# Optimization experiments

Hardware: AMD Instinct MI355X
Metric: run time of the kernel (lower is better)

## Reference

```python
import jax, jax.numpy as jnp
import numpy as np

N_NODES = 50000
N_EDGES = 800000
IN_DIM = 1024
HID = 512          # hidden_channels * heads, heads=1
N_CLASSES = 6
N_GRAPHS = 8
NEG_SLOPE = 0.2    # PyG GATConv default LeakyReLU slope
EPS = 1e-16


def gat_conv(x, W, att_src, att_dst, bias, src, dst):
    """PyG GATConv with heads=1, concat=True.
    x: [N, Fin], W: [Fin, C], att_src/att_dst: [C], bias: [C],
    src/dst: [E] (edge_index[0], edge_index[1]); messages flow src -> dst.
    """
    h = x @ W                                   # [N, C]
    a_s = h @ att_src                           # [N]
    a_d = h @ att_dst                           # [N]
    e = jax.nn.leaky_relu(a_s[src] + a_d[dst], NEG_SLOPE)   # [E]
    # segment softmax over destination node
    m = jax.ops.segment_max(e, dst, num_segments=N_NODES)   # [N]
    ex = jnp.exp(e - m[dst])                                 # [E]
    denom = jax.ops.segment_sum(ex, dst, num_segments=N_NODES)  # [N]
    alpha = ex / (denom[dst] + EPS)                           # [E]
    msg = alpha[:, None] * h[src]                             # [E, C]
    out = jax.ops.segment_sum(msg, dst, num_segments=N_NODES)  # [N, C]
    return out + bias


def setup_inputs() -> dict:
    key = jax.random.key(0)
    ks = jax.random.split(key, 20)
    x = jax.random.normal(ks[0], (N_NODES, IN_DIM), dtype=jnp.float32)
    edge_index = jax.random.randint(ks[1], (2, N_EDGES), 0, N_NODES, dtype=jnp.int32)
    batch = jnp.sort(jax.random.randint(ks[2], (N_NODES,), 0, N_GRAPHS, dtype=jnp.int32))

    def glorot(k, shape):
        fan = shape[0] + shape[-1]
        return jax.random.normal(k, shape, dtype=jnp.float32) * jnp.sqrt(2.0 / fan)

    inp = {"x": x, "edge_index": edge_index, "batch": batch}
    dims = [(IN_DIM, HID), (HID, HID), (HID, HID)]
    for i, (fi, fo) in enumerate(dims, start=1):
        inp[f"W{i}"] = glorot(ks[3 * i], (fi, fo))
        inp[f"as{i}"] = glorot(ks[3 * i + 1], (fo,))
        inp[f"ad{i}"] = glorot(ks[3 * i + 2], (fo,))
        inp[f"b{i}"] = jnp.zeros((fo,), dtype=jnp.float32)
    inp["Wlin"] = glorot(ks[13], (HID, N_CLASSES))
    inp["blin"] = jnp.zeros((N_CLASSES,), dtype=jnp.float32)
    return inp


def reference(x, W1, as1, ad1, b1, W2, as2, ad2, b2, W3, as3, ad3, b3,
              Wlin, blin, edge_index, batch):
    src, dst = edge_index[0], edge_index[1]
    h = gat_conv(x, W1, as1, ad1, b1, src, dst)
    h = jax.nn.relu(h)
    h = gat_conv(h, W2, as2, ad2, b2, src, dst)
    h = jax.nn.relu(h)
    h = gat_conv(h, W3, as3, ad3, b3, src, dst)
    # global_max_pool over graphs; dropout is identity in eval mode
    pooled = jax.ops.segment_max(h, batch, num_segments=N_GRAPHS)  # [G, HID]
    return pooled @ Wlin + blin                                     # [G, num_classes]
```

## Files before the change

kernel.cpp:

```cpp
#include <hip/hip_runtime.h>
#include <cmath>

#define N_NODES 50000
#define N_EDGES 800000
#define IN_DIM 1024
#define HID 512
#define N_CLASSES 6
#define N_GRAPHS 8
#define NEG_SLOPE 0.2f
#define SCAN_BLK 256
#define N_SCAN_BLOCKS ((N_NODES + SCAN_BLK - 1) / SCAN_BLK)
#define POOL_STRIP 256
#define POOL_NBLOCKS ((N_NODES + POOL_STRIP - 1) / POOL_STRIP)

typedef _Float16 half8 __attribute__((ext_vector_type(8)));
typedef _Float16 half4 __attribute__((ext_vector_type(4)));
typedef float floatx4 __attribute__((ext_vector_type(4)));

typedef const __attribute__((address_space(1))) void* gas_ptr;
typedef __attribute__((address_space(3))) void* las_ptr;
#define GLOAD16(gp, lp) \
    __builtin_amdgcn_global_load_lds((gas_ptr)(gp), (las_ptr)(lp), 16, 0, 0)

__global__ __launch_bounds__(256) void cast_x_f16(const float* __restrict__ x,
                                                  _Float16* __restrict__ x16) {
    const size_t TOT = (size_t)N_NODES * IN_DIM;
    size_t i = ((size_t)blockIdx.x * blockDim.x + threadIdx.x) * 8;
    const size_t step = (size_t)gridDim.x * blockDim.x * 8;
    for (; i < TOT; i += step) {
        float4 f0 = *(const float4*)(x + i);
        float4 f1 = *(const float4*)(x + i + 4);
        half8 o;
        o[0] = (_Float16)f0.x; o[1] = (_Float16)f0.y;
        o[2] = (_Float16)f0.z; o[3] = (_Float16)f0.w;
        o[4] = (_Float16)f1.x; o[5] = (_Float16)f1.y;
        o[6] = (_Float16)f1.z; o[7] = (_Float16)f1.w;
        *(half8*)(x16 + i) = o;
    }
}

__global__ __launch_bounds__(256) void transpose_cast_W3(const float* __restrict__ W1,
                                                         const float* __restrict__ W2,
                                                         const float* __restrict__ W3,
                                                         _Float16* __restrict__ Wt1,
                                                         _Float16* __restrict__ Wt2,
                                                         _Float16* __restrict__ Wt3) {
    const int l = blockIdx.z;
    const float* W = (l == 0) ? W1 : (l == 1) ? W2 : W3;
    _Float16* Wt   = (l == 0) ? Wt1 : (l == 1) ? Wt2 : Wt3;
    const int K    = (l == 0) ? IN_DIM : HID;
    if (blockIdx.x * 32 >= K) return;
    __shared__ float sh[32][33];
    const int kb = blockIdx.x * 32, nb = blockIdx.y * 32;
    const int tx = threadIdx.x & 31, ty = threadIdx.x >> 5;
#pragma unroll
    for (int i = 0; i < 32; i += 8)
        sh[ty + i][tx] = W[(size_t)(kb + ty + i) * HID + nb + tx];
    __syncthreads();
#pragma unroll
    for (int i = 0; i < 32; i += 8)
        Wt[(size_t)(nb + ty + i) * K + kb + tx] = (_Float16)sh[tx][ty + i];
}

__global__ __launch_bounds__(256) void gemm_mfma_f16(const _Float16* __restrict__ A,
                                                     const _Float16* __restrict__ Bt,
                                                     _Float16* __restrict__ C,
                                                     int M, int K) {
    const int nwg = gridDim.x;
    const int bid = blockIdx.x;
    const int q = nwg >> 3, r = nwg & 7;
    const int xcd = bid & 7, local = bid >> 3;
    const int wgid = (xcd < r) ? xcd * (q + 1) + local
                               : r * (q + 1) + (xcd - r) * q + local;
    const int rowBase = (wgid >> 2) * 128;
    const int colBase = (wgid & 3) * 128;

    const int tid  = threadIdx.x;
    const int lane = tid & 63;
    const int wave = tid >> 6;
    const int wm = wave >> 1, wn = wave & 1;

    __shared__ __align__(16) _Float16 As[128 * 64];
    __shared__ __align__(16) _Float16 Bs[128 * 64];

    const int fr = lane & 15;
    const int kc = lane >> 4;

    floatx4 acc[4][4] = {};

    const int lrow   = lane >> 3;
    const int gchunk = ((lane & 7) ^ lrow) * 8;
    const _Float16* aS[4];
    const _Float16* bS[4];
    _Float16* aD[4];
    _Float16* bD[4];
#pragma unroll
    for (int i = 0; i < 4; ++i) {
        int rr = wave * 32 + i * 8;
        int ar = rowBase + rr + lrow; if (ar > M - 1) ar = M - 1;
        aS[i] = A  + (size_t)ar * K + gchunk;
        bS[i] = Bt + (size_t)(colBase + rr + lrow) * K + gchunk;
        aD[i] = As + rr * 64;
        bD[i] = Bs + rr * 64;
    }

    const int cp0 = ((kc)     ^ (fr & 7)) * 8;
    const int cp1 = ((4 + kc) ^ (fr & 7)) * 8;
    const int aro = (wm * 64 + fr) * 64;
    const int bro = (wn * 64 + fr) * 64;

    for (int kb = 0; kb < K; kb += 64) {
#pragma unroll
        for (int i = 0; i < 4; ++i) {
            GLOAD16(aS[i] + kb, aD[i]);
            GLOAD16(bS[i] + kb, bD[i]);
        }
        __syncthreads();

#pragma unroll
        for (int kks = 0; kks < 2; ++kks) {
            const int cp = kks ? cp1 : cp0;
            half8 afr[4], bfr[4];
#pragma unroll
            for (int mi = 0; mi < 4; ++mi)
                afr[mi] = *(const half8*)&As[aro + mi * 1024 + cp];
#pragma unroll
            for (int ni = 0; ni < 4; ++ni)
                bfr[ni] = *(const half8*)&Bs[bro + ni * 1024 + cp];
#pragma unroll
            for (int mi = 0; mi < 4; ++mi)
#pragma unroll
                for (int ni = 0; ni < 4; ++ni)
                    acc[mi][ni] = __builtin_amdgcn_mfma_f32_16x16x32_f16(
                        afr[mi], bfr[ni], acc[mi][ni], 0, 0, 0);
        }
        __syncthreads();
    }

#pragma unroll
    for (int mi = 0; mi < 4; ++mi) {
#pragma unroll
        for (int ni = 0; ni < 4; ++ni) {
            int col = colBase + wn * 64 + ni * 16 + fr;
#pragma unroll
            for (int j = 0; j < 4; ++j) {
                int row = rowBase + wm * 64 + mi * 16 + kc * 4 + j;
                if (row < M) C[(size_t)row * HID + col] = (_Float16)acc[mi][ni][j];
            }
        }
    }
}

__global__ __launch_bounds__(256) void adot_kernel(const _Float16* __restrict__ h,
                                                   const float* __restrict__ att_s,
                                                   const float* __restrict__ att_d,
                                                   float* __restrict__ a_s,
                                                   float* __restrict__ a_d) {
    int wave = threadIdx.x >> 6;
    int lane = threadIdx.x & 63;
    int n = blockIdx.x * 4 + wave;
    if (n >= N_NODES) return;
    half8 hv = *(const half8*)(h + (size_t)n * HID + lane * 8);
    float4 s0 = ((const float4*)att_s)[lane * 2];
    float4 s1 = ((const float4*)att_s)[lane * 2 + 1];
    float4 d0 = ((const float4*)att_d)[lane * 2];
    float4 d1 = ((const float4*)att_d)[lane * 2 + 1];
    float hf[8];
#pragma unroll
    for (int q = 0; q < 8; ++q) hf[q] = (float)hv[q];
    float ss = hf[0]*s0.x + hf[1]*s0.y + hf[2]*s0.z + hf[3]*s0.w
             + hf[4]*s1.x + hf[5]*s1.y + hf[6]*s1.z + hf[7]*s1.w;
    float sd = hf[0]*d0.x + hf[1]*d0.y + hf[2]*d0.z + hf[3]*d0.w
             + hf[4]*d1.x + hf[5]*d1.y + hf[6]*d1.z + hf[7]*d1.w;
#pragma unroll
    for (int off = 32; off; off >>= 1) {
        ss += __shfl_down(ss, off);
        sd += __shfl_down(sd, off);
    }
    if (lane == 0) { a_s[n] = ss; a_d[n] = sd; }
}

__global__ void count_kernel(const int* __restrict__ dst, int* __restrict__ cnt) {
    int i = blockIdx.x * blockDim.x + threadIdx.x;
    if (i < N_EDGES) atomicAdd(cnt + dst[i], 1);
}

__global__ __launch_bounds__(SCAN_BLK) void scan1_kernel(const int* __restrict__ cnt,
                                                         int* __restrict__ partial,
                                                         int* __restrict__ blocksum) {
    __shared__ int tmp[SCAN_BLK];
    int t = threadIdx.x;
    int i = blockIdx.x * SCAN_BLK + t;
    int v = (i < N_NODES) ? cnt[i] : 0;
    tmp[t] = v;
    __syncthreads();
    for (int off = 1; off < SCAN_BLK; off <<= 1) {
        int u = (t >= off) ? tmp[t - off] : 0;
        __syncthreads();
        tmp[t] += u;
        __syncthreads();
    }
    if (i < N_NODES) partial[i] = tmp[t] - v;
    if (t == SCAN_BLK - 1) blocksum[blockIdx.x] = tmp[t];
}

__global__ __launch_bounds__(SCAN_BLK) void scan2_kernel(int* __restrict__ blocksum) {
    __shared__ int tmp[SCAN_BLK];
    int t = threadIdx.x;
    int v = (t < N_SCAN_BLOCKS) ? blocksum[t] : 0;
    tmp[t] = v;
    __syncthreads();
    for (int off = 1; off < SCAN_BLK; off <<= 1) {
        int u = (t >= off) ? tmp[t - off] : 0;
        __syncthreads();
        tmp[t] += u;
        __syncthreads();
    }
    if (t < N_SCAN_BLOCKS) blocksum[t] = tmp[t] - v;
}

__global__ __launch_bounds__(SCAN_BLK) void scan3_kernel(const int* __restrict__ partial,
                                                         const int* __restrict__ blocksum,
                                                         int* __restrict__ rowptr,
                                                         int* __restrict__ cursor) {
    int i = blockIdx.x * SCAN_BLK + threadIdx.x;
    if (i < N_NODES) {
        int r = partial[i] + blocksum[blockIdx.x];
        rowptr[i] = r;
        cursor[i] = r;
    }
    if (i == 0) rowptr[N_NODES] = N_EDGES;
}

__global__ void scatter_kernel(const int* __restrict__ src, const int* __restrict__ dst,
                               int* __restrict__ cursor, int* __restrict__ src_s) {
    int i = blockIdx.x * blockDim.x + threadIdx.x;
    if (i >= N_EDGES) return;
    int p = atomicAdd(cursor + dst[i], 1);
    src_s[p] = src[i];
}

__global__ __launch_bounds__(256) void alpha_kernel(const int* __restrict__ rowptr,
                                                    const int* __restrict__ src_s,
                                                    const float* __restrict__ a_s,
                                                    const float* __restrict__ a_d,
                                                    float* __restrict__ alpha) {
    const int grp = threadIdx.x >> 4;
    const int l16 = threadIdx.x & 15;
    const int n = blockIdx.x * 16 + grp;
    if (n >= N_NODES) return;
    const int beg = rowptr[n], end = rowptr[n + 1];
    const float a_dn = a_d[n];

    float vmax = -__builtin_inff();
    for (int j = beg + l16; j < end; j += 16) {
        float v = a_s[src_s[j]] + a_dn;
        v = v > 0.f ? v : NEG_SLOPE * v;
        alpha[j] = v;
        vmax = fmaxf(vmax, v);
    }
#pragma unroll
    for (int m = 1; m < 16; m <<= 1) vmax = fmaxf(vmax, __shfl_xor(vmax, m));

    float psum = 0.f;
    for (int j = beg + l16; j < end; j += 16) {
        float p = __expf(alpha[j] - vmax);
        alpha[j] = p;
        psum += p;
    }
#pragma unroll
    for (int m = 1; m < 16; m <<= 1) psum += __shfl_xor(psum, m);

    const float inv = 1.f / (psum + 1e-16f);
    for (int j = beg + l16; j < end; j += 16) alpha[j] *= inv;
}

__global__ __launch_bounds__(256) void aggregate2(const int* __restrict__ rowptr,
                                                  const int* __restrict__ src_s,
                                                  const float* __restrict__ alpha,
                                                  const _Float16* __restrict__ h,
                                                  const float* __restrict__ bias,
                                                  int do_relu,
                                                  _Float16* __restrict__ outx) {
    int wave = threadIdx.x >> 6;
    int lane = threadIdx.x & 63;
    int n = blockIdx.x * 4 + wave;
    if (n >= N_NODES) return;
    const int beg = rowptr[n], end = rowptr[n + 1];
    float acc[8] = {};
    int j = beg;
    for (; j + 1 < end; j += 2) {
        int s0 = src_s[j], s1 = src_s[j + 1];
        float al0 = alpha[j], al1 = alpha[j + 1];
        half8 hv0 = *(const half8*)(h + (size_t)s0 * HID + lane * 8);
        half8 hv1 = *(const half8*)(h + (size_t)s1 * HID + lane * 8);
#pragma unroll
        for (int q = 0; q < 8; ++q) acc[q] = fmaf(al0, (float)hv0[q], acc[q]);
#pragma unroll
        for (int q = 0; q < 8; ++q) acc[q] = fmaf(al1, (float)hv1[q], acc[q]);
    }
    if (j < end) {
        int s0 = src_s[j];
        float al0 = alpha[j];
        half8 hv0 = *(const half8*)(h + (size_t)s0 * HID + lane * 8);
#pragma unroll
        for (int q = 0; q < 8; ++q) acc[q] = fmaf(al0, (float)hv0[q], acc[q]);
    }
    const float4 b0 = ((const float4*)(bias + lane * 8))[0];
    const float4 b1 = ((const float4*)(bias + lane * 8))[1];
    float o[8];
    o[0] = acc[0] + b0.x; o[1] = acc[1] + b0.y;
    o[2] = acc[2] + b0.z; o[3] = acc[3] + b0.w;
    o[4] = acc[4] + b1.x; o[5] = acc[5] + b1.y;
    o[6] = acc[6] + b1.z; o[7] = acc[7] + b1.w;
    half8 ov;
#pragma unroll
    for (int q = 0; q < 8; ++q) {
        float val = do_relu ? fmaxf(o[q], 0.f) : o[q];
        ov[q] = (_Float16)val;
    }
    *(half8*)(outx + (size_t)n * HID + lane * 8) = ov;
}

__global__ __launch_bounds__(128) void pool1_kernel(const _Float16* __restrict__ X,
                                                    const int* __restrict__ batch,
                                                    float* __restrict__ partial) {
    const int t = threadIdx.x;
    const int b = blockIdx.x;
    const int n0 = b * POOL_STRIP;
    const int n1 = min(n0 + POOL_STRIP, N_NODES);
    const float NEG = -__builtin_inff();
    const float4 neg4 = make_float4(NEG, NEG, NEG, NEG);
#pragma unroll
    for (int g = 0; g < N_GRAPHS; ++g)
        ((float4*)(partial + ((size_t)b * N_GRAPHS + g) * HID))[t] = neg4;
    int gcur = batch[n0];
    float4 m = neg4;
    for (int n = n0; n < n1; ++n) {
        int g = batch[n];
        if (g != gcur) {
            ((float4*)(partial + ((size_t)b * N_GRAPHS + gcur) * HID))[t] = m;
            m = neg4;
            gcur = g;
        }
        half4 hv = *(const half4*)(X + (size_t)n * HID + t * 4);
        m.x = fmaxf(m.x, (float)hv[0]); m.y = fmaxf(m.y, (float)hv[1]);
        m.z = fmaxf(m.z, (float)hv[2]); m.w = fmaxf(m.w, (float)hv[3]);
    }
    ((float4*)(partial + ((size_t)b * N_GRAPHS + gcur) * HID))[t] = m;
}

__global__ __launch_bounds__(128) void pool2_kernel(const float* __restrict__ partial,
                                                    float* __restrict__ pooled) {
    const int g = blockIdx.x;
    const int t = threadIdx.x;
    const float NEG = -__builtin_inff();
    float4 m = make_float4(NEG, NEG, NEG, NEG);
    for (int b = 0; b < POOL_NBLOCKS; ++b) {
        float4 v = ((const float4*)(partial + ((size_t)b * N_GRAPHS + g) * HID))[t];
        m.x = fmaxf(m.x, v.x); m.y = fmaxf(m.y, v.y);
        m.z = fmaxf(m.z, v.z); m.w = fmaxf(m.w, v.w);
    }
    ((float4*)(pooled + (size_t)g * HID))[t] = m;
}

__global__ __launch_bounds__(64) void final_linear_kernel(const float* __restrict__ pooled,
                                                          const float* __restrict__ Wlin,
                                                          const float* __restrict__ blin,
                                                          float* __restrict__ out) {
    int t = threadIdx.x;
    if (t >= N_GRAPHS * N_CLASSES) return;
    int g = t / N_CLASSES, c = t % N_CLASSES;
    float s = blin[c];
    for (int k = 0; k < HID; ++k)
        s = fmaf(pooled[(size_t)g * HID + k], Wlin[(size_t)k * N_CLASSES + c], s);
    out[t] = s;
}

extern "C" void kernel_launch(void* const* d_in, const int* in_sizes, int n_in,
                              void* d_out, int out_size, void* d_ws, size_t ws_size,
                              hipStream_t stream) {
    const float* x       = (const float*)d_in[0];
    const int*   eidx    = (const int*)d_in[1];
    const int*   batch   = (const int*)d_in[2];
    const float* W[3]    = {(const float*)d_in[3], (const float*)d_in[7], (const float*)d_in[11]};
    const float* Asrc[3] = {(const float*)d_in[4], (const float*)d_in[8], (const float*)d_in[12]};
    const float* Adst[3] = {(const float*)d_in[5], (const float*)d_in[9], (const float*)d_in[13]};
    const float* Bias[3] = {(const float*)d_in[6], (const float*)d_in[10], (const float*)d_in[14]};
    const float* Wlin    = (const float*)d_in[15];
    const float* blin    = (const float*)d_in[16];
    const int* src = eidx;
    const int* dst = eidx + N_EDGES;

    float* wsf    = (float*)d_ws;
    _Float16* x16 = (_Float16*)wsf;
    float* ealpha = wsf + 24800000;
    _Float16* hH  = (_Float16*)(wsf + 25600000);
    _Float16* xAct= (_Float16*)(wsf + 25600000 + 12800000);
    float* a_s    = wsf + 25600000 + 12800000 + 12800000;
    float* a_d    = a_s + N_NODES;
    float* pooled = a_d + N_NODES;
    int* cnt      = (int*)(pooled + N_GRAPHS * HID);
    int* rowptr   = cnt + N_NODES;
    int* cursor   = rowptr + N_NODES + 1;
    int* partial  = cursor + N_NODES;
    int* blocksum = partial + N_NODES;
    int* src_s    = blocksum + 256;
    _Float16* Wt1 = (_Float16*)(src_s + N_EDGES);
    _Float16* Wt2 = Wt1 + (size_t)HID * IN_DIM;
    _Float16* Wt3 = Wt2 + (size_t)HID * HID;
    _Float16* WtL[3] = {Wt1, Wt2, Wt3};

    int edge_blocks = (N_EDGES + 255) / 256;

    hipMemsetAsync(cnt, 0, N_NODES * sizeof(int), stream);
    count_kernel<<<edge_blocks, 256, 0, stream>>>(dst, cnt);
    scan1_kernel<<<N_SCAN_BLOCKS, SCAN_BLK, 0, stream>>>(cnt, partial, blocksum);
    scan2_kernel<<<1, SCAN_BLK, 0, stream>>>(blocksum);
    scan3_kernel<<<N_SCAN_BLOCKS, SCAN_BLK, 0, stream>>>(partial, blocksum, rowptr, cursor);
    scatter_kernel<<<edge_blocks, 256, 0, stream>>>(src, dst, cursor, src_s);

    cast_x_f16<<<2048, 256, 0, stream>>>(x, x16);
    dim3 tgrid(IN_DIM / 32, HID / 32, 3);
    transpose_cast_W3<<<tgrid, 256, 0, stream>>>(W[0], W[1], W[2], Wt1, Wt2, Wt3);

    const int nrow_tiles = (N_NODES + 127) / 128;
    const int gemm_blocks = nrow_tiles * (HID / 128);
    for (int l = 0; l < 3; ++l) {
        int K = (l == 0) ? IN_DIM : HID;
        const _Float16* Ain = (l == 0) ? x16 : xAct;
        gemm_mfma_f16<<<gemm_blocks, 256, 0, stream>>>(Ain, WtL[l], hH, N_NODES, K);
        adot_kernel<<<(N_NODES + 3) / 4, 256, 0, stream>>>(hH, Asrc[l], Adst[l], a_s, a_d);
        alpha_kernel<<<(N_NODES + 15) / 16, 256, 0, stream>>>(rowptr, src_s, a_s, a_d, ealpha);
        aggregate2<<<(N_NODES + 3) / 4, 256, 0, stream>>>(
            rowptr, src_s, ealpha, hH, Bias[l], (l < 2) ? 1 : 0, xAct);
    }

    float* pool_partial = (float*)x16;
    pool1_kernel<<<POOL_NBLOCKS, 128, 0, stream>>>(xAct, batch, pool_partial);
    pool2_kernel<<<N_GRAPHS, 128, 0, stream>>>(pool_partial, pooled);
    final_linear_kernel<<<1, 64, 0, stream>>>(pooled, Wlin, blin, (float*)d_out);
}
```

Before: 830.3 us.

## Fuse attention dot products into GEMM epilogue and unroll aggregation by four

```diff
diff --git a/kernel.cpp b/kernel.cpp
--- a/kernel.cpp
+++ b/kernel.cpp
@@ -65,6 +65,10 @@
 __global__ __launch_bounds__(256) void gemm_mfma_f16(const _Float16* __restrict__ A,
                                                      const _Float16* __restrict__ Bt,
                                                      _Float16* __restrict__ C,
+                                                     const float* __restrict__ att_s,
+                                                     const float* __restrict__ att_d,
+                                                     float* __restrict__ a_s,
+                                                     float* __restrict__ a_d,
                                                      int M, int K) {
     const int nwg = gridDim.x;
     const int bid = blockIdx.x;
@@ -149,35 +153,36 @@
             }
         }
     }
-}
-
-__global__ __launch_bounds__(256) void adot_kernel(const _Float16* __restrict__ h,
-                                                   const float* __restrict__ att_s,
-                                                   const float* __restrict__ att_d,
-                                                   float* __restrict__ a_s,
-                                                   float* __restrict__ a_d) {
-    int wave = threadIdx.x >> 6;
-    int lane = threadIdx.x & 63;
-    int n = blockIdx.x * 4 + wave;
-    if (n >= N_NODES) return;
-    half8 hv = *(const half8*)(h + (size_t)n * HID + lane * 8);
-    float4 s0 = ((const float4*)att_s)[lane * 2];
-    float4 s1 = ((const float4*)att_s)[lane * 2 + 1];
-    float4 d0 = ((const float4*)att_d)[lane * 2];
-    float4 d1 = ((const float4*)att_d)[lane * 2 + 1];
-    float hf[8];
-#pragma unroll
-    for (int q = 0; q < 8; ++q) hf[q] = (float)hv[q];
-    float ss = hf[0]*s0.x + hf[1]*s0.y + hf[2]*s0.z + hf[3]*s0.w
-             + hf[4]*s1.x + hf[5]*s1.y + hf[6]*s1.z + hf[7]*s1.w;
-    float sd = hf[0]*d0.x + hf[1]*d0.y + hf[2]*d0.z + hf[3]*d0.w
-             + hf[4]*d1.x + hf[5]*d1.y + hf[6]*d1.z + hf[7]*d1.w;
-#pragma unroll
-    for (int off = 32; off; off >>= 1) {
-        ss += __shfl_down(ss, off);
-        sd += __shfl_down(sd, off);
-    }
-    if (lane == 0) { a_s[n] = ss; a_d[n] = sd; }
+
+    float as_c[4], ad_c[4];
+#pragma unroll
+    for (int ni = 0; ni < 4; ++ni) {
+        int col = colBase + wn * 64 + ni * 16 + fr;
+        as_c[ni] = att_s[col];
+        ad_c[ni] = att_d[col];
+    }
+#pragma unroll
+    for (int mi = 0; mi < 4; ++mi) {
+#pragma unroll
+        for (int j = 0; j < 4; ++j) {
+            float ps = acc[mi][0][j] * as_c[0] + acc[mi][1][j] * as_c[1]
+                     + acc[mi][2][j] * as_c[2] + acc[mi][3][j] * as_c[3];
+            float pd = acc[mi][0][j] * ad_c[0] + acc[mi][1][j] * ad_c[1]
+                     + acc[mi][2][j] * ad_c[2] + acc[mi][3][j] * ad_c[3];
+#pragma unroll
+            for (int mk = 1; mk < 16; mk <<= 1) {
+                ps += __shfl_xor(ps, mk);
+                pd += __shfl_xor(pd, mk);
+            }
+            if (fr == 0) {
+                int row = rowBase + wm * 64 + mi * 16 + kc * 4 + j;
+                if (row < M) {
+                    atomicAdd(a_s + row, ps);
+                    atomicAdd(a_d + row, pd);
+                }
+            }
+        }
+    }
 }
 
 __global__ void count_kernel(const int* __restrict__ dst, int* __restrict__ cnt) {
@@ -289,22 +294,28 @@
     const int beg = rowptr[n], end = rowptr[n + 1];
     float acc[8] = {};
     int j = beg;
-    for (; j + 1 < end; j += 2) {
-        int s0 = src_s[j], s1 = src_s[j + 1];
-        float al0 = alpha[j], al1 = alpha[j + 1];
+    for (; j + 3 < end; j += 4) {
+        int s0 = src_s[j], s1 = src_s[j + 1], s2 = src_s[j + 2], s3 = src_s[j + 3];
+        float al0 = alpha[j], al1 = alpha[j + 1], al2 = alpha[j + 2], al3 = alpha[j + 3];
         half8 hv0 = *(const half8*)(h + (size_t)s0 * HID + lane * 8);
         half8 hv1 = *(const half8*)(h + (size_t)s1 * HID + lane * 8);
-#pragma unroll
-        for (int q = 0; q < 8; ++q) acc[q] = fmaf(al0, (float)hv0[q], acc[q]);
-#pragma unroll
-        for (int q = 0; q < 8; ++q) acc[q] = fmaf(al1, (float)hv1[q], acc[q]);
-    }
-    if (j < end) {
+        half8 hv2 = *(const half8*)(h + (size_t)s2 * HID + lane * 8);
+        half8 hv3 = *(const half8*)(h + (size_t)s3 * HID + lane * 8);
+#pragma unroll
+        for (int qq = 0; qq < 8; ++qq) acc[qq] = fmaf(al0, (float)hv0[qq], acc[qq]);
+#pragma unroll
+        for (int qq = 0; qq < 8; ++qq) acc[qq] = fmaf(al1, (float)hv1[qq], acc[qq]);
+#pragma unroll
+        for (int qq = 0; qq < 8; ++qq) acc[qq] = fmaf(al2, (float)hv2[qq], acc[qq]);
+#pragma unroll
+        for (int qq = 0; qq < 8; ++qq) acc[qq] = fmaf(al3, (float)hv3[qq], acc[qq]);
+    }
+    for (; j < end; ++j) {
         int s0 = src_s[j];
         float al0 = alpha[j];
         half8 hv0 = *(const half8*)(h + (size_t)s0 * HID + lane * 8);
 #pragma unroll
-        for (int q = 0; q < 8; ++q) acc[q] = fmaf(al0, (float)hv0[q], acc[q]);
+        for (int qq = 0; qq < 8; ++qq) acc[qq] = fmaf(al0, (float)hv0[qq], acc[qq]);
     }
     const float4 b0 = ((const float4*)(bias + lane * 8))[0];
     const float4 b1 = ((const float4*)(bias + lane * 8))[1];
@@ -315,9 +326,9 @@
     o[6] = acc[6] + b1.z; o[7] = acc[7] + b1.w;
     half8 ov;
 #pragma unroll
-    for (int q = 0; q < 8; ++q) {
-        float val = do_relu ? fmaxf(o[q], 0.f) : o[q];
-        ov[q] = (_Float16)val;
+    for (int qq = 0; qq < 8; ++qq) {
+        float val = do_relu ? fmaxf(o[qq], 0.f) : o[qq];
+        ov[qq] = (_Float16)val;
     }
     *(half8*)(outx + (size_t)n * HID + lane * 8) = ov;
 }
@@ -429,8 +440,9 @@
     for (int l = 0; l < 3; ++l) {
         int K = (l == 0) ? IN_DIM : HID;
         const _Float16* Ain = (l == 0) ? x16 : xAct;
-        gemm_mfma_f16<<<gemm_blocks, 256, 0, stream>>>(Ain, WtL[l], hH, N_NODES, K);
-        adot_kernel<<<(N_NODES + 3) / 4, 256, 0, stream>>>(hH, Asrc[l], Adst[l], a_s, a_d);
+        hipMemsetAsync(a_s, 0, 2 * N_NODES * sizeof(float), stream);
+        gemm_mfma_f16<<<gemm_blocks, 256, 0, stream>>>(
+            Ain, WtL[l], hH, Asrc[l], Adst[l], a_s, a_d, N_NODES, K);
         alpha_kernel<<<(N_NODES + 15) / 16, 256, 0, stream>>>(rowptr, src_s, a_s, a_d, ealpha);
         aggregate2<<<(N_NODES + 3) / 4, 256, 0, stream>>>(
             rowptr, src_s, ealpha, hH, Bias[l], (l < 2) ? 1 : 0, xAct);
```

Result: slower. 853.5 us (+2.8%).

## Fuse fp32-to-fp16 input cast into layer-1 GEMM; unroll aggregation by four

Applied to the files above, without the earlier changes.

```diff
diff --git a/kernel.cpp b/kernel.cpp
--- a/kernel.cpp
+++ b/kernel.cpp
@@ -21,23 +21,6 @@
 typedef __attribute__((address_space(3))) void* las_ptr;
 #define GLOAD16(gp, lp) \
     __builtin_amdgcn_global_load_lds((gas_ptr)(gp), (las_ptr)(lp), 16, 0, 0)
-
-__global__ __launch_bounds__(256) void cast_x_f16(const float* __restrict__ x,
-                                                  _Float16* __restrict__ x16) {
-    const size_t TOT = (size_t)N_NODES * IN_DIM;
-    size_t i = ((size_t)blockIdx.x * blockDim.x + threadIdx.x) * 8;
-    const size_t step = (size_t)gridDim.x * blockDim.x * 8;
-    for (; i < TOT; i += step) {
-        float4 f0 = *(const float4*)(x + i);
-        float4 f1 = *(const float4*)(x + i + 4);
-        half8 o;
-        o[0] = (_Float16)f0.x; o[1] = (_Float16)f0.y;
-        o[2] = (_Float16)f0.z; o[3] = (_Float16)f0.w;
-        o[4] = (_Float16)f1.x; o[5] = (_Float16)f1.y;
-        o[6] = (_Float16)f1.z; o[7] = (_Float16)f1.w;
-        *(half8*)(x16 + i) = o;
-    }
-}
 
 __global__ __launch_bounds__(256) void transpose_cast_W3(const float* __restrict__ W1,
                                                          const float* __restrict__ W2,
@@ -62,10 +45,12 @@
         Wt[(size_t)(nb + ty + i) * K + kb + tx] = (_Float16)sh[tx][ty + i];
 }
 
-__global__ __launch_bounds__(256) void gemm_mfma_f16(const _Float16* __restrict__ A,
-                                                     const _Float16* __restrict__ Bt,
-                                                     _Float16* __restrict__ C,
-                                                     int M, int K) {
+template <typename AT>
+__global__ __launch_bounds__(256) void gemm_mfma(const AT* __restrict__ A,
+                                                 const _Float16* __restrict__ Bt,
+                                                 _Float16* __restrict__ C,
+                                                 int M, int K) {
+    constexpr bool F32A = (sizeof(AT) == 4);
     const int nwg = gridDim.x;
     const int bid = blockIdx.x;
     const int q = nwg >> 3, r = nwg & 7;
@@ -80,7 +65,7 @@
     const int wave = tid >> 6;
     const int wm = wave >> 1, wn = wave & 1;
 
-    __shared__ __align__(16) _Float16 As[128 * 64];
+    __shared__ __align__(16) AT       As[128 * 64];
     __shared__ __align__(16) _Float16 Bs[128 * 64];
 
     const int fr = lane & 15;
@@ -88,45 +73,92 @@
 
     floatx4 acc[4][4] = {};
 
-    const int lrow   = lane >> 3;
-    const int gchunk = ((lane & 7) ^ lrow) * 8;
-    const _Float16* aS[4];
+    constexpr int NA = F32A ? 8 : 4;
+    const AT* aS[NA];
+    AT*       aD[NA];
     const _Float16* bS[4];
-    _Float16* aD[4];
-    _Float16* bD[4];
-#pragma unroll
-    for (int i = 0; i < 4; ++i) {
-        int rr = wave * 32 + i * 8;
-        int ar = rowBase + rr + lrow; if (ar > M - 1) ar = M - 1;
-        aS[i] = A  + (size_t)ar * K + gchunk;
-        bS[i] = Bt + (size_t)(colBase + rr + lrow) * K + gchunk;
-        aD[i] = As + rr * 64;
-        bD[i] = Bs + rr * 64;
-    }
-
-    const int cp0 = ((kc)     ^ (fr & 7)) * 8;
-    const int cp1 = ((4 + kc) ^ (fr & 7)) * 8;
+    _Float16*       bD[4];
+    if constexpr (F32A) {
+        const int lrow = lane >> 4;
+#pragma unroll
+        for (int i = 0; i < 8; ++i) {
+            int rr = wave * 32 + i * 4;
+            int rowt = rr + lrow;
+            int ch = (lane & 15) ^ (rowt & 15);
+            int ar = rowBase + rowt; if (ar > M - 1) ar = M - 1;
+            aS[i] = A + (size_t)ar * K + ch * 4;
+            aD[i] = As + rr * 64;
+        }
+    } else {
+        const int lrow = lane >> 3;
+#pragma unroll
+        for (int i = 0; i < 4; ++i) {
+            int rr = wave * 32 + i * 8;
+            int ch = (lane & 7) ^ ((rr + lrow) & 7);
+            int ar = rowBase + rr + lrow; if (ar > M - 1) ar = M - 1;
+            aS[i] = A + (size_t)ar * K + ch * 8;
+            aD[i] = As + rr * 64;
+        }
+    }
+    {
+        const int lrow = lane >> 3;
+#pragma unroll
+        for (int i = 0; i < 4; ++i) {
+            int rr = wave * 32 + i * 8;
+            int ch = (lane & 7) ^ ((rr + lrow) & 7);
+            bS[i] = Bt + (size_t)(colBase + rr + lrow) * K + ch * 8;
+            bD[i] = Bs + rr * 64;
+        }
+    }
+
     const int aro = (wm * 64 + fr) * 64;
     const int bro = (wn * 64 + fr) * 64;
+    const int bcp0 = ((kc)     ^ (fr & 7)) * 8;
+    const int bcp1 = ((4 + kc) ^ (fr & 7)) * 8;
+    const int ac00 = ((2 * kc)     ^ fr) * 4;
+    const int ac01 = ((2 * kc + 1) ^ fr) * 4;
+    const int ac10 = ((8 + 2 * kc)     ^ fr) * 4;
+    const int ac11 = ((8 + 2 * kc + 1) ^ fr) * 4;
 
     for (int kb = 0; kb < K; kb += 64) {
-#pragma unroll
-        for (int i = 0; i < 4; ++i) {
-            GLOAD16(aS[i] + kb, aD[i]);
-            GLOAD16(bS[i] + kb, bD[i]);
-        }
+        if constexpr (F32A) {
+#pragma unroll
+            for (int i = 0; i < 8; ++i) GLOAD16(aS[i] + kb, aD[i]);
+        } else {
+#pragma unroll
+            for (int i = 0; i < 4; ++i) GLOAD16(aS[i] + kb, aD[i]);
+        }
+#pragma unroll
+        for (int i = 0; i < 4; ++i) GLOAD16(bS[i] + kb, bD[i]);
         __syncthreads();
 
 #pragma unroll
         for (int kks = 0; kks < 2; ++kks) {
-            const int cp = kks ? cp1 : cp0;
             half8 afr[4], bfr[4];
-#pragma unroll
-            for (int mi = 0; mi < 4; ++mi)
-                afr[mi] = *(const half8*)&As[aro + mi * 1024 + cp];
+            if constexpr (F32A) {
+                const int c0 = kks ? ac10 : ac00;
+                const int c1 = kks ? ac11 : ac01;
+#pragma unroll
+                for (int mi = 0; mi < 4; ++mi) {
+                    floatx4 f0 = *(const floatx4*)&As[aro + mi * 1024 + c0];
+                    floatx4 f1 = *(const floatx4*)&As[aro + mi * 1024 + c1];
+                    half8 h;
+                    h[0] = (_Float16)f0[0]; h[1] = (_Float16)f0[1];
+                    h[2] = (_Float16)f0[2]; h[3] = (_Float16)f0[3];
+                    h[4] = (_Float16)f1[0]; h[5] = (_Float16)f1[1];
+                    h[6] = (_Float16)f1[2]; h[7] = (_Float16)f1[3];
+                    afr[mi] = h;
+                }
+            } else {
+                const int cp = kks ? bcp1 : bcp0;
+#pragma unroll
+                for (int mi = 0; mi < 4; ++mi)
+                    afr[mi] = *(const half8*)&((const _Float16*)As)[aro + mi * 1024 + cp];
+            }
+            const int bcp = kks ? bcp1 : bcp0;
 #pragma unroll
             for (int ni = 0; ni < 4; ++ni)
-                bfr[ni] = *(const half8*)&Bs[bro + ni * 1024 + cp];
+                bfr[ni] = *(const half8*)&Bs[bro + ni * 1024 + bcp];
 #pragma unroll
             for (int mi = 0; mi < 4; ++mi)
 #pragma unroll
@@ -167,7 +199,7 @@
     float4 d1 = ((const float4*)att_d)[lane * 2 + 1];
     float hf[8];
 #pragma unroll
-    for (int q = 0; q < 8; ++q) hf[q] = (float)hv[q];
+    for (int qq = 0; qq < 8; ++qq) hf[qq] = (float)hv[qq];
     float ss = hf[0]*s0.x + hf[1]*s0.y + hf[2]*s0.z + hf[3]*s0.w
              + hf[4]*s1.x + hf[5]*s1.y + hf[6]*s1.z + hf[7]*s1.w;
     float sd = hf[0]*d0.x + hf[1]*d0.y + hf[2]*d0.z + hf[3]*d0.w
@@ -289,22 +321,28 @@
     const int beg = rowptr[n], end = rowptr[n + 1];
     float acc[8] = {};
     int j = beg;
-    for (; j + 1 < end; j += 2) {
-        int s0 = src_s[j], s1 = src_s[j + 1];
-        float al0 = alpha[j], al1 = alpha[j + 1];
+    for (; j + 3 < end; j += 4) {
+        int s0 = src_s[j], s1 = src_s[j + 1], s2 = src_s[j + 2], s3 = src_s[j + 3];
+        float al0 = alpha[j], al1 = alpha[j + 1], al2 = alpha[j + 2], al3 = alpha[j + 3];
         half8 hv0 = *(const half8*)(h + (size_t)s0 * HID + lane * 8);
         half8 hv1 = *(const half8*)(h + (size_t)s1 * HID + lane * 8);
-#pragma unroll
-        for (int q = 0; q < 8; ++q) acc[q] = fmaf(al0, (float)hv0[q], acc[q]);
-#pragma unroll
-        for (int q = 0; q < 8; ++q) acc[q] = fmaf(al1, (float)hv1[q], acc[q]);
-    }
-    if (j < end) {
+        half8 hv2 = *(const half8*)(h + (size_t)s2 * HID + lane * 8);
+        half8 hv3 = *(const half8*)(h + (size_t)s3 * HID + lane * 8);
+#pragma unroll
+        for (int qq = 0; qq < 8; ++qq) acc[qq] = fmaf(al0, (float)hv0[qq], acc[qq]);
+#pragma unroll
+        for (int qq = 0; qq < 8; ++qq) acc[qq] = fmaf(al1, (float)hv1[qq], acc[qq]);
+#pragma unroll
+        for (int qq = 0; qq < 8; ++qq) acc[qq] = fmaf(al2, (float)hv2[qq], acc[qq]);
+#pragma unroll
+        for (int qq = 0; qq < 8; ++qq) acc[qq] = fmaf(al3, (float)hv3[qq], acc[qq]);
+    }
+    for (; j < end; ++j) {
         int s0 = src_s[j];
         float al0 = alpha[j];
         half8 hv0 = *(const half8*)(h + (size_t)s0 * HID + lane * 8);
 #pragma unroll
-        for (int q = 0; q < 8; ++q) acc[q] = fmaf(al0, (float)hv0[q], acc[q]);
+        for (int qq = 0; qq < 8; ++qq) acc[qq] = fmaf(al0, (float)hv0[qq], acc[qq]);
     }
     const float4 b0 = ((const float4*)(bias + lane * 8))[0];
     const float4 b1 = ((const float4*)(bias + lane * 8))[1];
@@ -315,9 +353,9 @@
     o[6] = acc[6] + b1.z; o[7] = acc[7] + b1.w;
     half8 ov;
 #pragma unroll
-    for (int q = 0; q < 8; ++q) {
-        float val = do_relu ? fmaxf(o[q], 0.f) : o[q];
-        ov[q] = (_Float16)val;
+    for (int qq = 0; qq < 8; ++qq) {
+        float val = do_relu ? fmaxf(o[qq], 0.f) : o[qq];
+        ov[qq] = (_Float16)val;
     }
     *(half8*)(outx + (size_t)n * HID + lane * 8) = ov;
 }
@@ -393,7 +431,6 @@
     const int* dst = eidx + N_EDGES;
 
     float* wsf    = (float*)d_ws;
-    _Float16* x16 = (_Float16*)wsf;
     float* ealpha = wsf + 24800000;
     _Float16* hH  = (_Float16*)(wsf + 25600000);
     _Float16* xAct= (_Float16*)(wsf + 25600000 + 12800000);
@@ -409,7 +446,6 @@
     _Float16* Wt1 = (_Float16*)(src_s + N_EDGES);
     _Float16* Wt2 = Wt1 + (size_t)HID * IN_DIM;
     _Float16* Wt3 = Wt2 + (size_t)HID * HID;
-    _Float16* WtL[3] = {Wt1, Wt2, Wt3};
 
     int edge_blocks = (N_EDGES + 255) / 256;
 
@@ -420,23 +456,24 @@
     scan3_kernel<<<N_SCAN_BLOCKS, SCAN_BLK, 0, stream>>>(partial, blocksum, rowptr, cursor);
     scatter_kernel<<<edge_blocks, 256, 0, stream>>>(src, dst, cursor, src_s);
 
-    cast_x_f16<<<2048, 256, 0, stream>>>(x, x16);
     dim3 tgrid(IN_DIM / 32, HID / 32, 3);
     transpose_cast_W3<<<tgrid, 256, 0, stream>>>(W[0], W[1], W[2], Wt1, Wt2, Wt3);
 
     const int nrow_tiles = (N_NODES + 127) / 128;
     const int gemm_blocks = nrow_tiles * (HID / 128);
     for (int l = 0; l < 3; ++l) {
-        int K = (l == 0) ? IN_DIM : HID;
-        const _Float16* Ain = (l == 0) ? x16 : xAct;
-        gemm_mfma_f16<<<gemm_blocks, 256, 0, stream>>>(Ain, WtL[l], hH, N_NODES, K);
+        if (l == 0)
+            gemm_mfma<float><<<gemm_blocks, 256, 0, stream>>>(x, Wt1, hH, N_NODES, IN_DIM);
+        else
+            gemm_mfma<_Float16><<<gemm_blocks, 256, 0, stream>>>(
+                xAct, (l == 1) ? Wt2 : Wt3, hH, N_NODES, HID);
         adot_kernel<<<(N_NODES + 3) / 4, 256, 0, stream>>>(hH, Asrc[l], Adst[l], a_s, a_d);
         alpha_kernel<<<(N_NODES + 15) / 16, 256, 0, stream>>>(rowptr, src_s, a_s, a_d, ealpha);
         aggregate2<<<(N_NODES + 3) / 4, 256, 0, stream>>>(
             rowptr, src_s, ealpha, hH, Bias[l], (l < 2) ? 1 : 0, xAct);
     }
 
-    float* pool_partial = (float*)x16;
+    float* pool_partial = wsf;
     pool1_kernel<<<POOL_NBLOCKS, 128, 0, stream>>>(xAct, batch, pool_partial);
     pool2_kernel<<<N_GRAPHS, 128, 0, stream>>>(pool_partial, pooled);
     final_linear_kernel<<<1, 64, 0, stream>>>(pooled, Wlin, blin, (float*)d_out);
```

Result: faster. 806.5 us (median of 3 runs) (-2.9%).
